# Kernel tuning notes

Measured on AMD Instinct MI355X. Metric: run time of the kernel, lower is better.

The kernel has to match this reference:

```python
import jax, jax.numpy as jnp
import numpy as np

N = 100000      # nodes
E = 1600000     # edges
G = 256         # graphs in the batch
D_IN = 128
H = 128
C = 10
EPS = 1e-5      # BatchNorm eps


def setup_inputs() -> dict:
    key = jax.random.key(0)
    ks = jax.random.split(key, 32)
    inp = {
        'x': jax.random.normal(ks[0], (N, D_IN), jnp.float32),
        'edge_index': jax.random.randint(ks[1], (2, E), 0, N, dtype=jnp.int64),
        'batch': jnp.sort(jax.random.randint(ks[2], (N,), 0, G, dtype=jnp.int64)),
        'w1': jax.random.normal(ks[3], (D_IN, H), jnp.float32) * 0.05,
        'b1': jax.random.normal(ks[4], (H,), jnp.float32) * 0.05,
        'w2': jax.random.normal(ks[5], (H, H), jnp.float32) * 0.05,
        'b2': jax.random.normal(ks[6], (H,), jnp.float32) * 0.05,
        'w3': jax.random.normal(ks[7], (H, H), jnp.float32) * 0.05,
        'b3': jax.random.normal(ks[8], (H,), jnp.float32) * 0.05,
        'g1': jax.random.uniform(ks[9], (H,), jnp.float32, 0.5, 1.5),
        'be1': jax.random.normal(ks[10], (H,), jnp.float32) * 0.05,
        'm1': jax.random.normal(ks[11], (H,), jnp.float32) * 0.05,
        'v1': jax.random.uniform(ks[12], (H,), jnp.float32, 0.5, 1.5),
        'g2': jax.random.uniform(ks[13], (H,), jnp.float32, 0.5, 1.5),
        'be2': jax.random.normal(ks[14], (H,), jnp.float32) * 0.05,
        'm2': jax.random.normal(ks[15], (H,), jnp.float32) * 0.05,
        'v2': jax.random.uniform(ks[16], (H,), jnp.float32, 0.5, 1.5),
        'g3': jax.random.uniform(ks[17], (H,), jnp.float32, 0.5, 1.5),
        'be3': jax.random.normal(ks[18], (H,), jnp.float32) * 0.05,
        'm3': jax.random.normal(ks[19], (H,), jnp.float32) * 0.05,
        'v3': jax.random.uniform(ks[20], (H,), jnp.float32, 0.5, 1.5),
        'fcw1': jax.random.normal(ks[21], (H, H // 2), jnp.float32) * 0.05,
        'fcb1': jax.random.normal(ks[22], (H // 2,), jnp.float32) * 0.05,
        'fcw2': jax.random.normal(ks[23], (H // 2, C), jnp.float32) * 0.05,
        'fcb2': jax.random.normal(ks[24], (C,), jnp.float32) * 0.05,
    }
    return inp


def _gcn_norm(edge_index, n_nodes):
    # add self loops (PyG GCNConv default) and compute D^-1/2 (A+I) D^-1/2 norms
    loop = jnp.arange(n_nodes, dtype=edge_index.dtype)
    src = jnp.concatenate([edge_index[0], loop])
    dst = jnp.concatenate([edge_index[1], loop])
    deg = jax.ops.segment_sum(jnp.ones_like(dst, dtype=jnp.float32), dst, num_segments=n_nodes)
    dinv = jnp.where(deg > 0, jax.lax.rsqrt(deg), 0.0)
    norm = dinv[src] * dinv[dst]  # [E+N]
    return src, dst, norm


def _gcn_conv(x, W, b, src, dst, norm, n_nodes):
    h = x @ W                                   # [N, H]
    msg = norm[:, None] * h[src]                # gather + scale, [E+N, H]
    return jax.ops.segment_sum(msg, dst, num_segments=n_nodes) + b


def _bn_eval(x, gamma, beta, mean, var):
    return (x - mean) * jax.lax.rsqrt(var + EPS) * gamma + beta


def reference(x, edge_index, batch, w1, b1, w2, b2, w3, b3,
              g1, be1, m1, v1, g2, be2, m2, v2, g3, be3, m3, v3,
              fcw1, fcb1, fcw2, fcb2):
    n = x.shape[0]
    x = jnp.nan_to_num(x, nan=0.0, posinf=1e6, neginf=-1e6)
    src, dst, norm = _gcn_norm(edge_index, n)

    h = jax.nn.relu(_bn_eval(_gcn_conv(x, w1, b1, src, dst, norm, n), g1, be1, m1, v1))
    h = jax.nn.relu(_bn_eval(_gcn_conv(h, w2, b2, src, dst, norm, n), g2, be2, m2, v2))
    h = jax.nn.relu(_bn_eval(_gcn_conv(h, w3, b3, src, dst, norm, n), g3, be3, m3, v3))

    # global_mean_pool over graphs
    sums = jax.ops.segment_sum(h, batch, num_segments=G)            # [G, H]
    cnts = jax.ops.segment_sum(jnp.ones((n,), h.dtype), batch, num_segments=G)
    pooled = sums / jnp.maximum(cnts, 1.0)[:, None]

    out = jax.nn.relu(pooled @ fcw1 + fcb1) @ fcw2 + fcb2           # [G, C]
    return out
```

## Files before the change

kernel.cpp:

```cpp
#include <hip/hip_runtime.h>
#include <math.h>

#define NN 100000
#define EE 1600000
#define GG 256
#define HH 128
#define BSH 8
#define NBK 391
#define PASSA_WG 391
#define CAPB 6144

typedef __attribute__((ext_vector_type(8))) short short8;
typedef __attribute__((ext_vector_type(4))) float f32x4;

union U4S8 { uint4 u; short8 s; };

static __device__ __forceinline__ unsigned bf16rne(float f) {
    const unsigned u = __float_as_uint(f);
    return (u + 0x7fffu + ((u >> 16) & 1u)) >> 16;
}
static __device__ __forceinline__ unsigned packbf(float a, float b) {
    return bf16rne(a) | (bf16rne(b) << 16);
}
static __device__ __forceinline__ float bflo(unsigned u) { return __uint_as_float(u << 16); }
static __device__ __forceinline__ float bfhi(unsigned u) { return __uint_as_float(u & 0xffff0000u); }

__global__ __launch_bounds__(256) void setup_k(
    const int* __restrict__ ei, const int* __restrict__ batch,
    const float* __restrict__ w1, const float* __restrict__ w2,
    const float* __restrict__ w3,
    const float* __restrict__ b1, const float* __restrict__ g1,
    const float* __restrict__ be1, const float* __restrict__ m1,
    const float* __restrict__ v1,
    const float* __restrict__ b2, const float* __restrict__ g2,
    const float* __restrict__ be2, const float* __restrict__ m2,
    const float* __restrict__ v2,
    const float* __restrict__ b3, const float* __restrict__ g3,
    const float* __restrict__ be3, const float* __restrict__ m3,
    const float* __restrict__ v3,
    unsigned* __restrict__ bt, float* __restrict__ sc, float* __restrict__ sh,
    int* __restrict__ cursor, float* __restrict__ psum, int* __restrict__ gcnt,
    int* __restrict__ flags) {
    const int id = blockIdx.x * 256 + threadIdx.x;
    if (id < 24576) {
        const int w = id >> 13;
        const int rem = id & 8191;
        const int n = rem >> 6;
        const int kk = rem & 63;
        const float* W = (w == 0) ? w1 : (w == 1) ? w2 : w3;
        bt[id] = packbf(W[(2 * kk) * HH + n], W[(2 * kk + 1) * HH + n]);
    } else if (id < 24704) {
        const int c = id - 24576;
        float s;
        s = g1[c] / sqrtf(v1[c] + 1e-5f);
        sc[c] = s;           sh[c] = (b1[c] - m1[c]) * s + be1[c];
        s = g2[c] / sqrtf(v2[c] + 1e-5f);
        sc[128 + c] = s;     sh[128 + c] = (b2[c] - m2[c]) * s + be2[c];
        s = g3[c] / sqrtf(v3[c] + 1e-5f);
        sc[256 + c] = s;     sh[256 + c] = (b3[c] - m3[c]) * s + be3[c];
    } else if (id < 25095) {
        const int b = id - 24704;
        cursor[b] = b * CAPB;
    } else if (id < 57863) {
        psum[id - 25095] = 0.0f;
    } else if (id < 58119) {
        gcnt[id - 57863] = 0;
    } else if (id == 58119) {
        int e64 = 1;
        for (int j = 0; j < 8; ++j) {
            if (ei[2 * EE - 1 - 2 * j] != 0) { e64 = 0; break; }
        }
        flags[0] = e64;
        flags[1] = (batch[NN - 1] == 0) ? 1 : 0;
    }
}
#define SETUP_GRID 228

__global__ __launch_bounds__(256) void passA_k(const int* __restrict__ ei,
                                               const int* __restrict__ flags,
                                               int* __restrict__ cursor,
                                               unsigned* __restrict__ pairs) {
    __shared__ int h[NBK];
    __shared__ int rbase[NBK];
    const int tid = threadIdx.x;
    for (int i = tid; i < NBK; i += 256) h[i] = 0;
    __syncthreads();
    const bool e64 = flags[0] != 0;
    const int base = blockIdx.x * 4096;
    int scache[16], dcache[16];
#pragma unroll
    for (int j = 0; j < 16; ++j) {
        const int e = base + j * 256 + tid;
        int s = -1, d = 0;
        if (e < EE) {
            s = e64 ? ei[2 * e] : ei[e];
            d = e64 ? ei[2 * (EE + e)] : ei[EE + e];
            atomicAdd(&h[d >> BSH], 1);
        }
        scache[j] = s; dcache[j] = d;
    }
    __syncthreads();
    for (int i = tid; i < NBK; i += 256) {
        const int c = h[i];
        rbase[i] = c ? atomicAdd(&cursor[i], c) : 0;
    }
    __syncthreads();
    for (int i = tid; i < NBK; i += 256) h[i] = 0;
    __syncthreads();
#pragma unroll
    for (int j = 0; j < 16; ++j) {
        const int s = scache[j];
        if (s >= 0) {
            const int d = dcache[j];
            const int b = d >> BSH;
            const int r = atomicAdd(&h[b], 1);
            pairs[rbase[b] + r] = ((unsigned)(d & 255) << 17) | (unsigned)s;
        }
    }
}

__global__ __launch_bounds__(256) void passB_k(const unsigned* __restrict__ pairs,
                                               const int* __restrict__ cursor,
                                               int* __restrict__ offs,
                                               int* __restrict__ degcnt,
                                               float* __restrict__ dinv,
                                               int* __restrict__ csr) {
    __shared__ unsigned pk[CAPB];
    __shared__ int cnt[256];
    __shared__ int loff[256];
    __shared__ int sc[256];
    const int tid = threadIdx.x;
    const int b = blockIdx.x;
    const int p0 = b * CAPB;
    const int np = cursor[b] - p0;
    const int nb0 = b << BSH;
    const int nnode = (NN - nb0 < 256) ? (NN - nb0) : 256;

    cnt[tid] = 0;
    __syncthreads();
    for (int i = tid; i < np; i += 256) {
        const unsigned p = pairs[p0 + i];
        pk[i] = p;
        atomicAdd(&cnt[p >> 17], 1);
    }
    __syncthreads();
    const int creal = cnt[tid];
    const int cpad = (tid < nnode) ? ((creal + 8) & ~7) : 0;
    sc[tid] = cpad;
    __syncthreads();
    for (int off = 1; off < 256; off <<= 1) {
        int t = (tid >= off) ? sc[tid - off] : 0;
        __syncthreads();
        sc[tid] += t;
        __syncthreads();
    }
    const int ex = sc[tid] - cpad;
    loff[tid] = ex;
    if (tid < nnode) {
        const int node = nb0 + tid;
        offs[node] = p0 + ex;
        degcnt[node] = creal;
        dinv[node] = 1.0f / sqrtf((float)(creal + 1));
    }
    __syncthreads();
    cnt[tid] = 0;
    __syncthreads();
    for (int i = tid; i < np; i += 256) {
        const unsigned p = pk[i];
        const int dl = (int)(p >> 17);
        const int r = atomicAdd(&cnt[dl], 1);
        csr[p0 + loff[dl] + r] = (int)(p & 0x1FFFFu);
    }
    if (tid < nnode) {
        const int basep = p0 + loff[tid];
        csr[basep + creal] = nb0 + tid;
        for (int j = creal + 1; j < cpad; ++j) csr[basep + j] = NN;
    }
}

static __device__ __forceinline__ float sani(float v) {
    if (isnan(v)) return 0.0f;
    if (isinf(v)) return v > 0.0f ? 1e6f : -1e6f;
    return v;
}

__global__ __launch_bounds__(256) void gemm_mfma_k(const float* __restrict__ Af,
                                                   const unsigned* __restrict__ btg,
                                                   const float* __restrict__ dinv,
                                                   unsigned* __restrict__ C, int M) {
    __shared__ unsigned lds_u[8704];
    const int tid = threadIdx.x;
    const int wave = tid >> 6;
    const int lane = tid & 63;
    const int nl = lane & 15;
    const int q = lane >> 4;
    const int row0 = blockIdx.x * 64 + wave * 16;
    const int rowg = row0 + nl;
    const int rowa = min(rowg, M - 1);

    {
        const uint4* __restrict__ bg4 = (const uint4*)btg;
        for (int i = tid; i < 2048; i += 256) {
            const int n = i >> 4, w4 = i & 15;
            *(uint4*)&lds_u[n * 68 + w4 * 4] = bg4[n * 16 + w4];
        }
    }

    short8 a[4];
#pragma unroll
    for (int ks = 0; ks < 4; ++ks) {
        const float4 p = *(const float4*)(Af + (size_t)rowa * HH + ks * 32 + q * 8);
        const float4 r = *(const float4*)(Af + (size_t)rowa * HH + ks * 32 + q * 8 + 4);
        U4S8 cv;
        cv.u = make_uint4(packbf(sani(p.x), sani(p.y)), packbf(sani(p.z), sani(p.w)),
                          packbf(sani(r.x), sani(r.y)), packbf(sani(r.z), sani(r.w)));
        a[ks] = cv.s;
    }

    __syncthreads();

    f32x4 acc[8];
#pragma unroll
    for (int t = 0; t < 8; ++t) acc[t] = (f32x4)0.0f;

    const unsigned short* __restrict__ bts = (const unsigned short*)lds_u;
#pragma unroll
    for (int ks = 0; ks < 4; ++ks) {
#pragma unroll
        for (int t = 0; t < 8; ++t) {
            const int n = t * 16 + nl;
            const short8 b = *(const short8*)(bts + n * 136 + ks * 32 + q * 8);
            acc[t] = __builtin_amdgcn_mfma_f32_16x16x32_bf16(b, a[ks], acc[t], 0, 0, 0);
        }
    }

    if (rowg < M) {
        const float dsc = dinv[rowg];
        unsigned* crow = C + (size_t)rowg * 64;
#pragma unroll
        for (int t = 0; t < 8; ++t) {
            uint2 o;
            o.x = packbf(dsc * acc[t][0], dsc * acc[t][1]);
            o.y = packbf(dsc * acc[t][2], dsc * acc[t][3]);
            *(uint2*)(crow + t * 8 + q * 2) = o;
        }
    } else if (rowg == M) {
        unsigned* crow = C + (size_t)M * 64;
#pragma unroll
        for (int t = 0; t < 8; ++t)
            *(uint2*)(crow + t * 8 + q * 2) = make_uint2(0u, 0u);
    }
}

static __device__ __forceinline__ void gather4(
    const char* __restrict__ hb, const int* __restrict__ csr,
    const int st[4], const int np[4], const int maxp,
    const int sub, const unsigned cgo, float acc[4][8]) {
    int ia[4], ib[4];
#pragma unroll
    for (int i = 0; i < 4; ++i) {
        ia[i] = csr[st[i] + sub];
        ib[i] = csr[st[i] + 4 + sub];
    }
    for (int e = 0; e < maxp; e += 8) {
        uint4 r[8];
#pragma unroll
        for (int i = 0; i < 4; ++i) {
            const bool act = (e < np[i]);
            const unsigned sA = act ? (unsigned)ia[i] : (unsigned)NN;
            const unsigned sB = act ? (unsigned)ib[i] : (unsigned)NN;
            r[2 * i]     = *(const uint4*)(hb + ((sA << 8) | cgo));
            r[2 * i + 1] = *(const uint4*)(hb + ((sB << 8) | cgo));
        }
#pragma unroll
        for (int i = 0; i < 4; ++i) {
            ia[i] = csr[st[i] + e + 8 + sub];
            ib[i] = csr[st[i] + e + 12 + sub];
        }
#pragma unroll
        for (int i = 0; i < 4; ++i) {
            const uint4 rA = r[2 * i];
            const uint4 rB = r[2 * i + 1];
            acc[i][0] += bflo(rA.x) + bflo(rB.x);
            acc[i][1] += bfhi(rA.x) + bfhi(rB.x);
            acc[i][2] += bflo(rA.y) + bflo(rB.y);
            acc[i][3] += bfhi(rA.y) + bfhi(rB.y);
            acc[i][4] += bflo(rA.z) + bflo(rB.z);
            acc[i][5] += bfhi(rA.z) + bfhi(rB.z);
            acc[i][6] += bflo(rA.w) + bflo(rB.w);
            acc[i][7] += bfhi(rA.w) + bfhi(rB.w);
        }
    }
}

__global__ __launch_bounds__(256) void agg_gemm_k(
    const unsigned* __restrict__ hin, const int* __restrict__ csr,
    const int* __restrict__ offs, const int* __restrict__ cnt,
    const float* __restrict__ dinv,
    const float* __restrict__ bnsc, const float* __restrict__ bnsh,
    const unsigned* __restrict__ btg,
    unsigned* __restrict__ hout) {
    __shared__ unsigned ybuf[16 * 68];
    const int tid = threadIdx.x;
    const int wave = tid >> 6;
    const int lane = tid & 63;
    const int cg = lane & 15;
    const int sub = lane >> 4;
    const int c8 = cg * 8;
    const char* __restrict__ hb = (const char*)hin;
    const unsigned cgo = (unsigned)(cg << 4);

    if (blockIdx.x == 0 && tid < 64) hout[(size_t)NN * 64 + tid] = 0u;

    int st[4], np[4];
    float dvv[4];
#pragma unroll
    for (int i = 0; i < 4; ++i) {
        const int v = __builtin_amdgcn_readfirstlane(blockIdx.x * 16 + wave * 4 + i);
        st[i] = offs[v];
        np[i] = (cnt[v] + 8) & ~7;
        dvv[i] = dinv[v];
    }
    const int maxp = max(max(np[0], np[1]), max(np[2], np[3]));

    float acc[4][8];
#pragma unroll
    for (int i = 0; i < 4; ++i)
#pragma unroll
        for (int j = 0; j < 8; ++j) acc[i][j] = 0.0f;

    gather4(hb, csr, st, np, maxp, sub, cgo, acc);

    const float4 sca = *(const float4*)(bnsc + c8);
    const float4 scb = *(const float4*)(bnsc + c8 + 4);
    const float4 sha = *(const float4*)(bnsh + c8);
    const float4 shb = *(const float4*)(bnsh + c8 + 4);

#pragma unroll
    for (int i = 0; i < 4; ++i) {
#pragma unroll
        for (int j = 0; j < 8; ++j) {
            acc[i][j] += __shfl_xor(acc[i][j], 16);
            acc[i][j] += __shfl_xor(acc[i][j], 32);
        }
        if (sub == 0) {
            const float dv = dvv[i];
            const float y0 = fmaxf(dv * acc[i][0] * sca.x + sha.x, 0.0f);
            const float y1 = fmaxf(dv * acc[i][1] * sca.y + sha.y, 0.0f);
            const float y2 = fmaxf(dv * acc[i][2] * sca.z + sha.z, 0.0f);
            const float y3 = fmaxf(dv * acc[i][3] * sca.w + sha.w, 0.0f);
            const float y4 = fmaxf(dv * acc[i][4] * scb.x + shb.x, 0.0f);
            const float y5 = fmaxf(dv * acc[i][5] * scb.y + shb.y, 0.0f);
            const float y6 = fmaxf(dv * acc[i][6] * scb.z + shb.z, 0.0f);
            const float y7 = fmaxf(dv * acc[i][7] * scb.w + shb.w, 0.0f);
            *(uint4*)&ybuf[(wave * 4 + i) * 68 + cg * 4] =
                make_uint4(packbf(y0, y1), packbf(y2, y3), packbf(y4, y5), packbf(y6, y7));
        }
    }
    __syncthreads();

    const int nl = cg;
    const int q = sub;
    short8 arow[4];
#pragma unroll
    for (int ks = 0; ks < 4; ++ks) {
        U4S8 cv;
        cv.u = *(const uint4*)&ybuf[nl * 68 + ks * 16 + q * 4];
        arow[ks] = cv.s;
    }
    const uint4* __restrict__ bt4 = (const uint4*)btg;
    const int t0 = wave * 2;
    f32x4 acc0 = (f32x4)0.0f, acc1 = (f32x4)0.0f;
#pragma unroll
    for (int ks = 0; ks < 4; ++ks) {
        U4S8 b0, b1;
        b0.u = bt4[((t0 + 0) * 16 + nl) * 16 + ks * 4 + q];
        b1.u = bt4[((t0 + 1) * 16 + nl) * 16 + ks * 4 + q];
        acc0 = __builtin_amdgcn_mfma_f32_16x16x32_bf16(b0.s, arow[ks], acc0, 0, 0, 0);
        acc1 = __builtin_amdgcn_mfma_f32_16x16x32_bf16(b1.s, arow[ks], acc1, 0, 0, 0);
    }
    const int rowg = blockIdx.x * 16 + nl;
    const float dsc = dinv[rowg];
    unsigned* crow = hout + (size_t)rowg * 64;
    uint2 o0, o1;
    o0.x = packbf(dsc * acc0[0], dsc * acc0[1]);
    o0.y = packbf(dsc * acc0[2], dsc * acc0[3]);
    o1.x = packbf(dsc * acc1[0], dsc * acc1[1]);
    o1.y = packbf(dsc * acc1[2], dsc * acc1[3]);
    *(uint2*)(crow + (t0 + 0) * 8 + q * 2) = o0;
    *(uint2*)(crow + (t0 + 1) * 8 + q * 2) = o1;
}

__global__ __launch_bounds__(256) void agg_pool_k(
    const unsigned* __restrict__ hpre, const int* __restrict__ csr,
    const int* __restrict__ offs, const int* __restrict__ cnt,
    const float* __restrict__ dinv,
    const float* __restrict__ bnsc, const float* __restrict__ bnsh,
    const int* __restrict__ batch, const int* __restrict__ flags,
    float* __restrict__ psum, int* __restrict__ gcnt) {
    __shared__ float yb[16][128];
    __shared__ int gid[16];
    const int tid = threadIdx.x;
    const int wave = tid >> 6;
    const int lane = tid & 63;
    const int cg = lane & 15;
    const int sub = lane >> 4;
    const int c8 = cg * 8;
    const char* __restrict__ hb = (const char*)hpre;
    const unsigned cgo = (unsigned)(cg << 4);
    const bool b64 = flags[1] != 0;

    int st[4], np[4];
    float dvv[4];
#pragma unroll
    for (int i = 0; i < 4; ++i) {
        const int v = __builtin_amdgcn_readfirstlane(blockIdx.x * 16 + wave * 4 + i);
        st[i] = offs[v];
        np[i] = (cnt[v] + 8) & ~7;
        dvv[i] = dinv[v];
        if (lane == 0) gid[wave * 4 + i] = b64 ? batch[2 * v] : batch[v];
    }
    const int maxp = max(max(np[0], np[1]), max(np[2], np[3]));

    float acc[4][8];
#pragma unroll
    for (int i = 0; i < 4; ++i)
#pragma unroll
        for (int j = 0; j < 8; ++j) acc[i][j] = 0.0f;

    gather4(hb, csr, st, np, maxp, sub, cgo, acc);

    const float4 sca = *(const float4*)(bnsc + c8);
    const float4 scb = *(const float4*)(bnsc + c8 + 4);
    const float4 sha = *(const float4*)(bnsh + c8);
    const float4 shb = *(const float4*)(bnsh + c8 + 4);

#pragma unroll
    for (int i = 0; i < 4; ++i) {
#pragma unroll
        for (int j = 0; j < 8; ++j) {
            acc[i][j] += __shfl_xor(acc[i][j], 16);
            acc[i][j] += __shfl_xor(acc[i][j], 32);
        }
        if (sub == 0) {
            const float dv = dvv[i];
            const int row = wave * 4 + i;
            yb[row][c8 + 0] = fmaxf(dv * acc[i][0] * sca.x + sha.x, 0.0f);
            yb[row][c8 + 1] = fmaxf(dv * acc[i][1] * sca.y + sha.y, 0.0f);
            yb[row][c8 + 2] = fmaxf(dv * acc[i][2] * sca.z + sha.z, 0.0f);
            yb[row][c8 + 3] = fmaxf(dv * acc[i][3] * sca.w + sha.w, 0.0f);
            yb[row][c8 + 4] = fmaxf(dv * acc[i][4] * scb.x + shb.x, 0.0f);
            yb[row][c8 + 5] = fmaxf(dv * acc[i][5] * scb.y + shb.y, 0.0f);
            yb[row][c8 + 6] = fmaxf(dv * acc[i][6] * scb.z + shb.z, 0.0f);
            yb[row][c8 + 7] = fmaxf(dv * acc[i][7] * scb.w + shb.w, 0.0f);
        }
    }
    __syncthreads();

    if (tid < 128) {
        float s = 0.0f;
        int cur = gid[0];
        for (int r = 0; r < 16; ++r) {
            const int g = gid[r];
            if (g != cur) {
                atomicAdd(&psum[cur * HH + tid], s);
                cur = g; s = 0.0f;
            }
            s += yb[r][tid];
        }
        atomicAdd(&psum[cur * HH + tid], s);
    } else if (tid == 128) {
        int cur = gid[0], c = 0;
        for (int r = 0; r < 16; ++r) {
            const int g = gid[r];
            if (g != cur) {
                atomicAdd(&gcnt[cur], c);
                cur = g; c = 0;
            }
            ++c;
        }
        atomicAdd(&gcnt[cur], c);
    }
}

__global__ __launch_bounds__(128) void head_k(
    const float* __restrict__ psum, const int* __restrict__ gcnt,
    const float* __restrict__ fw1, const float* __restrict__ fb1,
    const float* __restrict__ fw2, const float* __restrict__ fb2,
    float* __restrict__ out) {
    __shared__ float pooled[128];
    __shared__ float hid[64];
    const int g = blockIdx.x;
    const int tid = threadIdx.x;

    const int cntn = gcnt[g];
    pooled[tid] = psum[g * HH + tid] / (float)(cntn > 0 ? cntn : 1);
    __syncthreads();

    if (tid < 64) {
        float a = fb1[tid];
#pragma unroll 4
        for (int k = 0; k < 128; ++k) a += pooled[k] * fw1[k * 64 + tid];
        hid[tid] = fmaxf(a, 0.0f);
    }
    __syncthreads();
    if (tid < 10) {
        float a = fb2[tid];
#pragma unroll
        for (int k = 0; k < 64; ++k) a += hid[k] * fw2[k * 10 + tid];
        out[g * 10 + tid] = a;
    }
}

extern "C" void kernel_launch(void* const* d_in, const int* in_sizes, int n_in,
                              void* d_out, int out_size, void* d_ws, size_t ws_size,
                              hipStream_t stream) {
    const float* x_in  = (const float*)d_in[0];
    const int*   ei    = (const int*)d_in[1];
    const int*   batch = (const int*)d_in[2];
    const float* w1 = (const float*)d_in[3];
    const float* b1 = (const float*)d_in[4];
    const float* w2 = (const float*)d_in[5];
    const float* b2 = (const float*)d_in[6];
    const float* w3 = (const float*)d_in[7];
    const float* b3 = (const float*)d_in[8];
    const float* g1 = (const float*)d_in[9];
    const float* be1 = (const float*)d_in[10];
    const float* m1 = (const float*)d_in[11];
    const float* v1 = (const float*)d_in[12];
    const float* g2 = (const float*)d_in[13];
    const float* be2 = (const float*)d_in[14];
    const float* m2 = (const float*)d_in[15];
    const float* v2 = (const float*)d_in[16];
    const float* g3 = (const float*)d_in[17];
    const float* be3 = (const float*)d_in[18];
    const float* m3 = (const float*)d_in[19];
    const float* v3 = (const float*)d_in[20];
    const float* fw1 = (const float*)d_in[21];
    const float* fb1 = (const float*)d_in[22];
    const float* fw2 = (const float*)d_in[23];
    const float* fb2 = (const float*)d_in[24];
    float* out = (float*)d_out;

    size_t off = 0;
    char* base = (char*)d_ws;
    auto alloc = [&](size_t bytes) -> void* {
        void* p = base + off;
        off += (bytes + 255) & ~(size_t)255;
        return p;
    };
    int*      degcnt = (int*)alloc((size_t)NN * 4);
    float*    dinv   = (float*)alloc((size_t)NN * 4);
    int*      offs   = (int*)alloc((size_t)NN * 4);
    int*      cursor = (int*)alloc((size_t)NBK * 4);
    int*      flags  = (int*)alloc(256);
    float*    bnsc   = (float*)alloc(3 * 128 * 4);
    float*    bnsh   = (float*)alloc(3 * 128 * 4);
    unsigned* btg    = (unsigned*)alloc(3 * 8192 * 4);
    float*    psum   = (float*)alloc((size_t)GG * HH * 4);
    int*      gcnt   = (int*)alloc((size_t)GG * 4);
    int*      csr    = (int*)alloc((size_t)NBK * CAPB * 4);
    unsigned* pairs  = (unsigned*)alloc((size_t)NBK * CAPB * 4);
    unsigned* bufA   = (unsigned*)alloc((size_t)(NN + 1) * 64 * 4);
    unsigned* bufB   = (unsigned*)alloc((size_t)(NN + 1) * 64 * 4);
    if (off > ws_size) return;

    setup_k<<<SETUP_GRID, 256, 0, stream>>>(ei, batch, w1, w2, w3,
                                            b1, g1, be1, m1, v1,
                                            b2, g2, be2, m2, v2,
                                            b3, g3, be3, m3, v3,
                                            btg, bnsc, bnsh, cursor, psum, gcnt,
                                            flags);
    passA_k<<<PASSA_WG, 256, 0, stream>>>(ei, flags, cursor, pairs);
    passB_k<<<NBK, 256, 0, stream>>>(pairs, cursor, offs, degcnt, dinv, csr);

    const int ggrid = (NN + 63) / 64;
    const int fgrid = NN / 16;

    gemm_mfma_k<<<ggrid, 256, 0, stream>>>(x_in, btg, dinv, bufA, NN);
    agg_gemm_k<<<fgrid, 256, 0, stream>>>(bufA, csr, offs, degcnt, dinv,
                                          bnsc, bnsh, btg + 8192, bufB);
    agg_gemm_k<<<fgrid, 256, 0, stream>>>(bufB, csr, offs, degcnt, dinv,
                                          bnsc + 128, bnsh + 128, btg + 16384, bufA);
    agg_pool_k<<<fgrid, 256, 0, stream>>>(bufA, csr, offs, degcnt, dinv,
                                          bnsc + 256, bnsh + 256, batch, flags,
                                          psum, gcnt);
    head_k<<<GG, 128, 0, stream>>>(psum, gcnt, fw1, fb1, fw2, fb2, out);
}
```

Baseline: 408.9 us.

## Sort CSR neighbor lists in LDS and use packed float2 accumulation in gathers

The CSR build now assembles each bucket's adjacency in shared memory, insertion-sorts every node's source list, and then writes the bucket to global memory with coalesced stores. Sorted neighbor indices should give the gather kernels more locality in their row reads. The aggregation accumulators are also switched to two-wide float vectors so the compiler can emit packed FP32 adds. The cost is an extra 24KB of LDS in passB and a serial per-thread insertion sort whose time grows with node degree.

```diff
diff --git a/kernel.cpp b/kernel.cpp
--- a/kernel.cpp
+++ b/kernel.cpp
@@ -12,6 +12,7 @@
 
 typedef __attribute__((ext_vector_type(8))) short short8;
 typedef __attribute__((ext_vector_type(4))) float f32x4;
+typedef __attribute__((ext_vector_type(2))) float f32x2;
 
 union U4S8 { uint4 u; short8 s; };
 
@@ -24,6 +25,9 @@
 }
 static __device__ __forceinline__ float bflo(unsigned u) { return __uint_as_float(u << 16); }
 static __device__ __forceinline__ float bfhi(unsigned u) { return __uint_as_float(u & 0xffff0000u); }
+static __device__ __forceinline__ f32x2 up2(unsigned u) {
+    f32x2 r; r.x = bflo(u); r.y = bfhi(u); return r;
+}
 
 __global__ __launch_bounds__(256) void setup_k(
     const int* __restrict__ ei, const int* __restrict__ batch,
@@ -126,9 +130,11 @@
                                                float* __restrict__ dinv,
                                                int* __restrict__ csr) {
     __shared__ unsigned pk[CAPB];
+    __shared__ int lcs[CAPB];
     __shared__ int cnt[256];
     __shared__ int loff[256];
     __shared__ int sc[256];
+    __shared__ int tot;
     const int tid = threadIdx.x;
     const int b = blockIdx.x;
     const int p0 = b * CAPB;
@@ -156,6 +162,7 @@
     }
     const int ex = sc[tid] - cpad;
     loff[tid] = ex;
+    if (tid == 255) tot = sc[255];
     if (tid < nnode) {
         const int node = nb0 + tid;
         offs[node] = p0 + ex;
@@ -169,13 +176,25 @@
         const unsigned p = pk[i];
         const int dl = (int)(p >> 17);
         const int r = atomicAdd(&cnt[dl], 1);
-        csr[p0 + loff[dl] + r] = (int)(p & 0x1FFFFu);
-    }
+        lcs[loff[dl] + r] = (int)(p & 0x1FFFFu);
+    }
+    __syncthreads();
     if (tid < nnode) {
-        const int basep = p0 + loff[tid];
-        csr[basep + creal] = nb0 + tid;
-        for (int j = creal + 1; j < cpad; ++j) csr[basep + j] = NN;
-    }
+        const int b0 = loff[tid];
+        for (int j = 1; j < creal; ++j) {
+            const int key = lcs[b0 + j];
+            int k2 = j - 1;
+            while (k2 >= 0 && lcs[b0 + k2] > key) {
+                lcs[b0 + k2 + 1] = lcs[b0 + k2];
+                --k2;
+            }
+            lcs[b0 + k2 + 1] = key;
+        }
+        lcs[b0 + creal] = nb0 + tid;
+        for (int j = creal + 1; j < cpad; ++j) lcs[b0 + j] = NN;
+    }
+    __syncthreads();
+    for (int i = tid; i < tot; i += 256) csr[p0 + i] = lcs[i];
 }
 
 static __device__ __forceinline__ float sani(float v) {
@@ -255,7 +274,7 @@
 static __device__ __forceinline__ void gather4(
     const char* __restrict__ hb, const int* __restrict__ csr,
     const int st[4], const int np[4], const int maxp,
-    const int sub, const unsigned cgo, float acc[4][8]) {
+    const int sub, const unsigned cgo, f32x2 acc[4][4]) {
     int ia[4], ib[4];
 #pragma unroll
     for (int i = 0; i < 4; ++i) {
@@ -281,14 +300,10 @@
         for (int i = 0; i < 4; ++i) {
             const uint4 rA = r[2 * i];
             const uint4 rB = r[2 * i + 1];
-            acc[i][0] += bflo(rA.x) + bflo(rB.x);
-            acc[i][1] += bfhi(rA.x) + bfhi(rB.x);
-            acc[i][2] += bflo(rA.y) + bflo(rB.y);
-            acc[i][3] += bfhi(rA.y) + bfhi(rB.y);
-            acc[i][4] += bflo(rA.z) + bflo(rB.z);
-            acc[i][5] += bfhi(rA.z) + bfhi(rB.z);
-            acc[i][6] += bflo(rA.w) + bflo(rB.w);
-            acc[i][7] += bfhi(rA.w) + bfhi(rB.w);
+            acc[i][0] += up2(rA.x) + up2(rB.x);
+            acc[i][1] += up2(rA.y) + up2(rB.y);
+            acc[i][2] += up2(rA.z) + up2(rB.z);
+            acc[i][3] += up2(rA.w) + up2(rB.w);
         }
     }
 }
@@ -323,11 +338,11 @@
     }
     const int maxp = max(max(np[0], np[1]), max(np[2], np[3]));
 
-    float acc[4][8];
+    f32x2 acc[4][4];
 #pragma unroll
     for (int i = 0; i < 4; ++i)
 #pragma unroll
-        for (int j = 0; j < 8; ++j) acc[i][j] = 0.0f;
+        for (int j = 0; j < 4; ++j) acc[i][j] = (f32x2)0.0f;
 
     gather4(hb, csr, st, np, maxp, sub, cgo, acc);
 
@@ -339,20 +354,22 @@
 #pragma unroll
     for (int i = 0; i < 4; ++i) {
 #pragma unroll
-        for (int j = 0; j < 8; ++j) {
-            acc[i][j] += __shfl_xor(acc[i][j], 16);
-            acc[i][j] += __shfl_xor(acc[i][j], 32);
+        for (int j = 0; j < 4; ++j) {
+            acc[i][j].x += __shfl_xor(acc[i][j].x, 16);
+            acc[i][j].y += __shfl_xor(acc[i][j].y, 16);
+            acc[i][j].x += __shfl_xor(acc[i][j].x, 32);
+            acc[i][j].y += __shfl_xor(acc[i][j].y, 32);
         }
         if (sub == 0) {
             const float dv = dvv[i];
-            const float y0 = fmaxf(dv * acc[i][0] * sca.x + sha.x, 0.0f);
-            const float y1 = fmaxf(dv * acc[i][1] * sca.y + sha.y, 0.0f);
-            const float y2 = fmaxf(dv * acc[i][2] * sca.z + sha.z, 0.0f);
-            const float y3 = fmaxf(dv * acc[i][3] * sca.w + sha.w, 0.0f);
-            const float y4 = fmaxf(dv * acc[i][4] * scb.x + shb.x, 0.0f);
-            const float y5 = fmaxf(dv * acc[i][5] * scb.y + shb.y, 0.0f);
-            const float y6 = fmaxf(dv * acc[i][6] * scb.z + shb.z, 0.0f);
-            const float y7 = fmaxf(dv * acc[i][7] * scb.w + shb.w, 0.0f);
+            const float y0 = fmaxf(dv * acc[i][0].x * sca.x + sha.x, 0.0f);
+            const float y1 = fmaxf(dv * acc[i][0].y * sca.y + sha.y, 0.0f);
+            const float y2 = fmaxf(dv * acc[i][1].x * sca.z + sha.z, 0.0f);
+            const float y3 = fmaxf(dv * acc[i][1].y * sca.w + sha.w, 0.0f);
+            const float y4 = fmaxf(dv * acc[i][2].x * scb.x + shb.x, 0.0f);
+            const float y5 = fmaxf(dv * acc[i][2].y * scb.y + shb.y, 0.0f);
+            const float y6 = fmaxf(dv * acc[i][3].x * scb.z + shb.z, 0.0f);
+            const float y7 = fmaxf(dv * acc[i][3].y * scb.w + shb.w, 0.0f);
             *(uint4*)&ybuf[(wave * 4 + i) * 68 + cg * 4] =
                 make_uint4(packbf(y0, y1), packbf(y2, y3), packbf(y4, y5), packbf(y6, y7));
         }
@@ -422,11 +439,11 @@
     }
     const int maxp = max(max(np[0], np[1]), max(np[2], np[3]));
 
-    float acc[4][8];
+    f32x2 acc[4][4];
 #pragma unroll
     for (int i = 0; i < 4; ++i)
 #pragma unroll
-        for (int j = 0; j < 8; ++j) acc[i][j] = 0.0f;
+        for (int j = 0; j < 4; ++j) acc[i][j] = (f32x2)0.0f;
 
     gather4(hb, csr, st, np, maxp, sub, cgo, acc);
 
@@ -438,21 +455,23 @@
 #pragma unroll
     for (int i = 0; i < 4; ++i) {
 #pragma unroll
-        for (int j = 0; j < 8; ++j) {
-            acc[i][j] += __shfl_xor(acc[i][j], 16);
-            acc[i][j] += __shfl_xor(acc[i][j], 32);
+        for (int j = 0; j < 4; ++j) {
+            acc[i][j].x += __shfl_xor(acc[i][j].x, 16);
+            acc[i][j].y += __shfl_xor(acc[i][j].y, 16);
+            acc[i][j].x += __shfl_xor(acc[i][j].x, 32);
+            acc[i][j].y += __shfl_xor(acc[i][j].y, 32);
         }
         if (sub == 0) {
             const float dv = dvv[i];
             const int row = wave * 4 + i;
-            yb[row][c8 + 0] = fmaxf(dv * acc[i][0] * sca.x + sha.x, 0.0f);
-            yb[row][c8 + 1] = fmaxf(dv * acc[i][1] * sca.y + sha.y, 0.0f);
-            yb[row][c8 + 2] = fmaxf(dv * acc[i][2] * sca.z + sha.z, 0.0f);
-            yb[row][c8 + 3] = fmaxf(dv * acc[i][3] * sca.w + sha.w, 0.0f);
-            yb[row][c8 + 4] = fmaxf(dv * acc[i][4] * scb.x + shb.x, 0.0f);
-            yb[row][c8 + 5] = fmaxf(dv * acc[i][5] * scb.y + shb.y, 0.0f);
-            yb[row][c8 + 6] = fmaxf(dv * acc[i][6] * scb.z + shb.z, 0.0f);
-            yb[row][c8 + 7] = fmaxf(dv * acc[i][7] * scb.w + shb.w, 0.0f);
+            yb[row][c8 + 0] = fmaxf(dv * acc[i][0].x * sca.x + sha.x, 0.0f);
+            yb[row][c8 + 1] = fmaxf(dv * acc[i][0].y * sca.y + sha.y, 0.0f);
+            yb[row][c8 + 2] = fmaxf(dv * acc[i][1].x * sca.z + sha.z, 0.0f);
+            yb[row][c8 + 3] = fmaxf(dv * acc[i][1].y * sca.w + sha.w, 0.0f);
+            yb[row][c8 + 4] = fmaxf(dv * acc[i][2].x * scb.x + shb.x, 0.0f);
+            yb[row][c8 + 5] = fmaxf(dv * acc[i][2].y * scb.y + shb.y, 0.0f);
+            yb[row][c8 + 6] = fmaxf(dv * acc[i][3].x * scb.z + shb.z, 0.0f);
+            yb[row][c8 + 7] = fmaxf(dv * acc[i][3].y * scb.w + shb.w, 0.0f);
         }
     }
     __syncthreads();
```

Result: slower. 448.4 us (+9.7%).
